# Kernel tuning notes

Hardware: AMD Instinct MI355X
Metric: run time of the kernel (lower is better)

The kernel has to match this reference:

```python
import jax, jax.numpy as jnp
import numpy as np

EPS_RMS = 1e-6
EPS_Q = 1e-5
EPS_NORM = 1e-10


def _rmsnorm(x):
    return x * jax.lax.rsqrt(jnp.mean(x * x, axis=-1, keepdims=True) + EPS_RMS)


def _activation_quant(x):
    # per-token 8-bit absmax quantization (BitNet b1.58)
    scale = 127.0 / jnp.maximum(jnp.max(jnp.abs(x), axis=-1, keepdims=True), EPS_Q)
    return jnp.clip(jnp.round(x * scale), -128.0, 127.0) / scale


def _weight_quant(w):
    # per-tensor ternary quantization with mean-abs scale
    scale = 1.0 / jnp.maximum(jnp.mean(jnp.abs(w)), EPS_Q)
    return jnp.clip(jnp.round(w * scale), -1.0, 1.0) / scale


def _bitlinear(x, w, b):
    xn = _rmsnorm(x)
    xq = xn + jax.lax.stop_gradient(_activation_quant(xn) - xn)  # STE
    wq = w + jax.lax.stop_gradient(_weight_quant(w) - w)         # STE
    return jnp.einsum('bsf,of->bso', xq, wq) + b


def setup_inputs() -> dict:
    key = jax.random.key(0)
    ks = jax.random.split(key, 4)
    B, S, F = 32, 1024, 512
    evidence_features = jax.random.normal(ks[0], (B, S, F), dtype=jnp.float32)
    prior_belief = jax.random.uniform(ks[1], (B, S, F), dtype=jnp.float32)
    W1 = jax.random.normal(ks[2], (F, 2 * F), dtype=jnp.float32) * (1.0 / np.sqrt(2 * F))
    b1 = jnp.zeros((F,), dtype=jnp.float32)
    W2 = jax.random.normal(ks[3], (F, F), dtype=jnp.float32) * (1.0 / np.sqrt(F))
    b2 = jnp.zeros((F,), dtype=jnp.float32)
    return {"evidence_features": evidence_features, "prior_belief": prior_belief,
            "W1": W1, "b1": b1, "W2": W2, "b2": b2}


def reference(evidence_features, prior_belief, W1, b1, W2, b2):
    # belief_update MLP on concat(prior, evidence)
    update_input = jnp.concatenate([prior_belief, evidence_features], axis=-1)  # [B,S,2F]
    h = jax.nn.relu(_bitlinear(update_input, W1, b1))                           # [B,S,F]
    likelihood_factors = jax.nn.sigmoid(_bitlinear(h, W2, b2))                  # [B,S,F]
    posterior_unnorm = prior_belief * likelihood_factors
    normalizer = jnp.maximum(jnp.sum(posterior_unnorm, axis=1, keepdims=True), EPS_NORM)
    return posterior_unnorm / normalizer
```

## Files before the change

### kernel.cpp

```cpp
#include <hip/hip_runtime.h>
#include <math.h>

typedef __attribute__((ext_vector_type(4))) int i32x4;
typedef __attribute__((ext_vector_type(2))) int i32x2;
typedef __attribute__((ext_vector_type(4))) float f32x4;

#define GLOAD_LDS16(g, l)                                          \
  __builtin_amdgcn_global_load_lds(                                \
      (const __attribute__((address_space(1))) void*)(g),          \
      (__attribute__((address_space(3))) void*)(l), 16, 0, 0)

__global__ void kWabs(const float* __restrict__ w1, const float* __restrict__ w2,
                      double* __restrict__ part) {
  const bool second = blockIdx.x >= 256;
  const float* w = second ? w2 : w1;
  const int n = second ? 262144 : 524288;
  int t = (blockIdx.x & 255) * 256 + threadIdx.x;
  double s = 0.0;
  for (int i = t; i < n; i += 65536) s += (double)fabsf(w[i]);
#pragma unroll
  for (int m = 32; m >= 1; m >>= 1) s += __shfl_xor(s, m);
  __shared__ double sd[4];
  int lane = threadIdx.x & 63, wid = threadIdx.x >> 6;
  if (lane == 0) sd[wid] = s;
  __syncthreads();
  if (threadIdx.x == 0) part[blockIdx.x] = (sd[0] + sd[1]) + (sd[2] + sd[3]);
}

__global__ void kWfin(const double* __restrict__ part, float* __restrict__ wsv) {
  const double* p = part + blockIdx.x * 256;
  const double n = (blockIdx.x == 0) ? 524288.0 : 262144.0;
  double s = p[threadIdx.x];
#pragma unroll
  for (int m = 32; m >= 1; m >>= 1) s += __shfl_xor(s, m);
  __shared__ double sd[4];
  int lane = threadIdx.x & 63, wid = threadIdx.x >> 6;
  if (lane == 0) sd[wid] = s;
  __syncthreads();
  if (threadIdx.x == 0) {
    double tot = (sd[0] + sd[1]) + (sd[2] + sd[3]);
    wsv[blockIdx.x] = fmaxf((float)(tot / n), 1e-5f);
  }
}

__global__ void kWq(const float* __restrict__ w1, const float* __restrict__ w2,
                    const float* __restrict__ wsv,
                    char* __restrict__ wq1, char* __restrict__ wq2) {
  const bool second = blockIdx.x >= 2048;
  const float* w = second ? w2 : w1;
  char* wq = second ? wq2 : wq1;
  const float scale = 1.0f / wsv[second ? 1 : 0];
  int i = (second ? blockIdx.x - 2048 : blockIdx.x) * 256 + threadIdx.x;
  float q = fminf(fmaxf(rintf(w[i] * scale), -1.0f), 1.0f);
  wq[i] = (char)(int)q;
}

__global__ __launch_bounds__(512) void kQ1(
    const float* __restrict__ prior, const float* __restrict__ evid,
    char* __restrict__ Xq, float* __restrict__ rAct) {
  const int w = threadIdx.x >> 6;
  const int l = threadIdx.x & 63;
  const size_t row = (size_t)blockIdx.x * 8 + w;
  const f32x4* pp = (const f32x4*)(prior + row * 512) + l * 2;
  const f32x4* pe = (const f32x4*)(evid + row * 512) + l * 2;
  f32x4 x[4];
  x[0] = pp[0]; x[1] = pp[1]; x[2] = pe[0]; x[3] = pe[1];
  float ss = 0.f, mx = 0.f;
#pragma unroll
  for (int v = 0; v < 4; ++v)
#pragma unroll
    for (int i = 0; i < 4; ++i) { float f = x[v][i]; ss += f * f; mx = fmaxf(mx, fabsf(f)); }
#pragma unroll
  for (int m = 32; m >= 1; m >>= 1) { ss += __shfl_xor(ss, m); mx = fmaxf(mx, __shfl_xor(mx, m)); }
  const float inv = 1.0f / sqrtf(ss * (1.0f / 1024.0f) + 1e-6f);
  const float amax = fmaxf(mx * inv, 1e-5f);
  const float s = 127.0f / amax;
  int pk[4];
#pragma unroll
  for (int v = 0; v < 4; ++v) {
    int p = 0;
#pragma unroll
    for (int i = 0; i < 4; ++i) {
      int qi = (int)fminf(fmaxf(rintf(x[v][i] * inv * s), -128.0f), 127.0f);
      p |= (qi & 255) << (8 * i);
    }
    pk[v] = p;
  }
  char* dst = Xq + row * 1024 + l * 8;
  *(i32x2*)dst = (i32x2){pk[0], pk[1]};
  *(i32x2*)(dst + 512) = (i32x2){pk[2], pk[3]};
  if (l == 0) rAct[row] = amax / 127.0f;
}

template <int KDIM, bool L1>
__global__ __launch_bounds__(512, 4) void kGemm(
    const char* __restrict__ Xq, const char* __restrict__ Wq,
    const float* __restrict__ biasG, const float* __restrict__ rAct,
    const float* __restrict__ wS,
    char* __restrict__ XqOut, float* __restrict__ rActOut,
    const float* __restrict__ prior, float* __restrict__ outUn,
    float* __restrict__ partG) {
  struct Stage { char A[4096]; char B[32768]; };
  __shared__ __align__(16) union {
    Stage st[2];
    struct { float sq[64][8]; float mx[64][8]; } ep;
  } u;
  __shared__ float rowR[64];
  __shared__ float biasS[512];
  __shared__ float normPart[512];

  const int tid = threadIdx.x;
  const int lane = tid & 63;
  const int wn = tid >> 6;
  const int lr = lane & 15;
  const int kg = lane >> 4;
  const size_t row0 = (size_t)blockIdx.x * 64;

  if (tid < 64) rowR[tid] = rAct[row0 + tid];
  biasS[tid] = biasG[tid];

  i32x4 acc[4][4];
#pragma unroll
  for (int a = 0; a < 4; ++a)
#pragma unroll
    for (int b = 0; b < 4; ++b) acc[a][b] = (i32x4){0, 0, 0, 0};

  const int lrow = lane >> 2;
  const int lkb = (lane & 3) * 16;

  const char* gA = Xq + (row0 + (wn & 3) * 16 + lrow) * (size_t)KDIM + lkb;
  const char* gB[4];
#pragma unroll
  for (int r = 0; r < 4; ++r)
    gB[r] = Wq + ((wn * 4 + r) * 16 + lrow) * (size_t)KDIM + lkb;

#define STAGE(b, k0)                                                   \
  do {                                                                 \
    if (wn < 4) GLOAD_LDS16(gA + (k0), &u.st[b].A[(wn & 3) * 1024]);   \
    _Pragma("unroll")                                                  \
    for (int r = 0; r < 4; ++r)                                        \
      GLOAD_LDS16(gB[r] + (k0), &u.st[b].B[(wn * 4 + r) * 1024]);      \
  } while (0)

  constexpr int NT = KDIM / 64;
  STAGE(0, 0);
  __syncthreads();

#pragma unroll 2
  for (int kt = 0; kt < NT; ++kt) {
    const int cur = kt & 1;
    if (kt + 1 < NT) STAGE(cur ^ 1, (kt + 1) * 64);
    i32x4 af[4];
#pragma unroll
    for (int fm = 0; fm < 4; ++fm)
      af[fm] = *(const i32x4*)&u.st[cur].A[(fm * 16 + lr) * 64 + kg * 16];
#pragma unroll
    for (int fn = 0; fn < 4; ++fn) {
      i32x4 bf = *(const i32x4*)&u.st[cur].B[(wn * 64 + fn * 16 + lr) * 64 + kg * 16];
#pragma unroll
      for (int fm = 0; fm < 4; ++fm)
        acc[fm][fn] = __builtin_amdgcn_mfma_i32_16x16x64_i8(af[fm], bf, acc[fm][fn], 0, 0, 0);
    }
    __syncthreads();
  }
#undef STAGE

  const float wsv_ = wS[0];

  if constexpr (L1) {
    f32x4 fa[4][4];
#pragma unroll
    for (int fm = 0; fm < 4; ++fm) {
      float sc[4];
#pragma unroll
      for (int j = 0; j < 4; ++j) sc[j] = rowR[fm * 16 + kg * 4 + j] * wsv_;
#pragma unroll
      for (int fn = 0; fn < 4; ++fn) {
        const float bb = biasS[wn * 64 + fn * 16 + lr];
#pragma unroll
        for (int j = 0; j < 4; ++j)
          fa[fm][fn][j] = fmaxf((float)acc[fm][fn][j] * sc[j] + bb, 0.0f);
      }
    }
#pragma unroll
    for (int fm = 0; fm < 4; ++fm)
#pragma unroll
      for (int j = 0; j < 4; ++j) {
        float ss = 0.f, mx = 0.f;
#pragma unroll
        for (int fn = 0; fn < 4; ++fn) { float h = fa[fm][fn][j]; ss += h * h; mx = fmaxf(mx, h); }
#pragma unroll
        for (int m = 8; m >= 1; m >>= 1) { ss += __shfl_xor(ss, m); mx = fmaxf(mx, __shfl_xor(mx, m)); }
        if (lr == 0) {
          int rl = fm * 16 + kg * 4 + j;
          u.ep.sq[rl][wn] = ss;
          u.ep.mx[rl][wn] = mx;
        }
      }
    __syncthreads();
#pragma unroll
    for (int fm = 0; fm < 4; ++fm)
#pragma unroll
      for (int j = 0; j < 4; ++j) {
        const int rl = fm * 16 + kg * 4 + j;
        float sst = 0.f, mxt = 0.f;
#pragma unroll
        for (int w = 0; w < 8; ++w) {
          sst += u.ep.sq[rl][w];
          mxt = fmaxf(mxt, u.ep.mx[rl][w]);
        }
        float inv = 1.0f / sqrtf(sst * (1.0f / 512.0f) + 1e-6f);
        float amax = fmaxf(mxt * inv, 1e-5f);
        float s = 127.0f / amax;
        if (lr == 0 && wn == 0) rActOut[row0 + rl] = amax / 127.0f;
#pragma unroll
        for (int fn = 0; fn < 4; ++fn) {
          float xn = fa[fm][fn][j] * inv;
          int qi = (int)fminf(fmaxf(rintf(xn * s), -128.0f), 127.0f);
          XqOut[(row0 + rl) * 512 + wn * 64 + fn * 16 + lr] = (char)qi;
        }
      }
  } else {
    float colsum[4] = {0.f, 0.f, 0.f, 0.f};
#pragma unroll
    for (int fm = 0; fm < 4; ++fm) {
      float sc[4];
#pragma unroll
      for (int j = 0; j < 4; ++j) sc[j] = rowR[fm * 16 + kg * 4 + j] * wsv_;
#pragma unroll
      for (int fn = 0; fn < 4; ++fn) {
        const int col = wn * 64 + fn * 16 + lr;
        const float bb = biasS[col];
#pragma unroll
        for (int j = 0; j < 4; ++j) {
          const size_t rg = row0 + fm * 16 + kg * 4 + j;
          float v = (float)acc[fm][fn][j] * sc[j] + bb;
          float like = 1.0f / (1.0f + expf(-v));
          float un = prior[rg * 512 + col] * like;
          outUn[rg * 512 + col] = un;
          colsum[fn] += un;
        }
      }
    }
#pragma unroll
    for (int fn = 0; fn < 4; ++fn) {
      colsum[fn] += __shfl_xor(colsum[fn], 16);
      colsum[fn] += __shfl_xor(colsum[fn], 32);
    }
    if (lane < 16) {
#pragma unroll
      for (int fn = 0; fn < 4; ++fn) normPart[wn * 64 + fn * 16 + lane] = colsum[fn];
    }
    __syncthreads();
    partG[(size_t)blockIdx.x * 512 + tid] = normPart[tid];
  }
}

__global__ void kNorm1(const float* __restrict__ partG, float* __restrict__ normA) {
  const int b = blockIdx.x, f = threadIdx.x;
  float s = 0.f;
#pragma unroll
  for (int i = 0; i < 16; ++i) s += partG[(size_t)(b * 16 + i) * 512 + f];
  normA[b * 512 + f] = fmaxf(s, 1e-10f);
}

__global__ void kNorm2(float* __restrict__ out, const float* __restrict__ normA) {
  const size_t i4 = (size_t)blockIdx.x * blockDim.x + threadIdx.x;
  f32x4 v = ((const f32x4*)out)[i4];
  const int f4 = (int)(i4 & 127);
  const int b = (int)(i4 >> 17);
  f32x4 n = ((const f32x4*)normA)[b * 128 + f4];
  v[0] /= n[0]; v[1] /= n[1]; v[2] /= n[2]; v[3] /= n[3];
  ((f32x4*)out)[i4] = v;
}

extern "C" void kernel_launch(void* const* d_in, const int* in_sizes, int n_in,
                              void* d_out, int out_size, void* d_ws, size_t ws_size,
                              hipStream_t stream) {
  const float* evid  = (const float*)d_in[0];
  const float* prior = (const float*)d_in[1];
  const float* W1    = (const float*)d_in[2];
  const float* b1    = (const float*)d_in[3];
  const float* W2    = (const float*)d_in[4];
  const float* b2    = (const float*)d_in[5];
  float* out = (float*)d_out;

  char* ws = (char*)d_ws;
  char*   X2q   = ws;
  char*   W1q   = ws + 16777216;
  char*   W2q   = ws + 17301504;
  float*  r1    = (float*)(ws + 17563648);
  float*  r2    = (float*)(ws + 17694720);
  double* part  = (double*)(ws + 17825792);
  float*  wsv   = (float*)(ws + 17829888);
  float*  partG = (float*)(ws + 17830144);
  float*  normA = (float*)(ws + 18878720);

  char* X1q = (char*)d_out;

  kWabs<<<512, 256, 0, stream>>>(W1, W2, part);
  kWfin<<<2, 256, 0, stream>>>(part, wsv);
  kWq<<<3072, 256, 0, stream>>>(W1, W2, wsv, W1q, W2q);
  kQ1<<<4096, 512, 0, stream>>>(prior, evid, X1q, r1);
  kGemm<1024, true><<<512, 512, 0, stream>>>(X1q, W1q, b1, r1, wsv + 0,
                                             X2q, r2, nullptr, nullptr, nullptr);
  kGemm<512, false><<<512, 512, 0, stream>>>(X2q, W2q, b2, r2, wsv + 1,
                                             nullptr, nullptr, prior, out, partG);
  kNorm1<<<32, 512, 0, stream>>>(partG, normA);
  kNorm2<<<16384, 256, 0, stream>>>(out, normA);
}
```

Before: 131.8 us.

## Fuse first-layer activation quantization into the first GEMM via LDS-resident A tile

```diff
diff --git a/kernel.cpp b/kernel.cpp
--- a/kernel.cpp
+++ b/kernel.cpp
@@ -2,7 +2,6 @@
 #include <math.h>
 
 typedef __attribute__((ext_vector_type(4))) int i32x4;
-typedef __attribute__((ext_vector_type(2))) int i32x2;
 typedef __attribute__((ext_vector_type(4))) float f32x4;
 
 #define GLOAD_LDS16(g, l)                                          \
@@ -55,59 +54,18 @@
   wq[i] = (char)(int)q;
 }
 
-__global__ __launch_bounds__(512) void kQ1(
+__global__ __launch_bounds__(512, 1) void kFused1(
     const float* __restrict__ prior, const float* __restrict__ evid,
-    char* __restrict__ Xq, float* __restrict__ rAct) {
-  const int w = threadIdx.x >> 6;
-  const int l = threadIdx.x & 63;
-  const size_t row = (size_t)blockIdx.x * 8 + w;
-  const f32x4* pp = (const f32x4*)(prior + row * 512) + l * 2;
-  const f32x4* pe = (const f32x4*)(evid + row * 512) + l * 2;
-  f32x4 x[4];
-  x[0] = pp[0]; x[1] = pp[1]; x[2] = pe[0]; x[3] = pe[1];
-  float ss = 0.f, mx = 0.f;
-#pragma unroll
-  for (int v = 0; v < 4; ++v)
-#pragma unroll
-    for (int i = 0; i < 4; ++i) { float f = x[v][i]; ss += f * f; mx = fmaxf(mx, fabsf(f)); }
-#pragma unroll
-  for (int m = 32; m >= 1; m >>= 1) { ss += __shfl_xor(ss, m); mx = fmaxf(mx, __shfl_xor(mx, m)); }
-  const float inv = 1.0f / sqrtf(ss * (1.0f / 1024.0f) + 1e-6f);
-  const float amax = fmaxf(mx * inv, 1e-5f);
-  const float s = 127.0f / amax;
-  int pk[4];
-#pragma unroll
-  for (int v = 0; v < 4; ++v) {
-    int p = 0;
-#pragma unroll
-    for (int i = 0; i < 4; ++i) {
-      int qi = (int)fminf(fmaxf(rintf(x[v][i] * inv * s), -128.0f), 127.0f);
-      p |= (qi & 255) << (8 * i);
-    }
-    pk[v] = p;
-  }
-  char* dst = Xq + row * 1024 + l * 8;
-  *(i32x2*)dst = (i32x2){pk[0], pk[1]};
-  *(i32x2*)(dst + 512) = (i32x2){pk[2], pk[3]};
-  if (l == 0) rAct[row] = amax / 127.0f;
-}
-
-template <int KDIM, bool L1>
-__global__ __launch_bounds__(512, 4) void kGemm(
-    const char* __restrict__ Xq, const char* __restrict__ Wq,
-    const float* __restrict__ biasG, const float* __restrict__ rAct,
+    const char* __restrict__ Wq, const float* __restrict__ biasG,
     const float* __restrict__ wS,
-    char* __restrict__ XqOut, float* __restrict__ rActOut,
-    const float* __restrict__ prior, float* __restrict__ outUn,
-    float* __restrict__ partG) {
-  struct Stage { char A[4096]; char B[32768]; };
+    char* __restrict__ XqOut, float* __restrict__ rActOut) {
+  __shared__ __align__(16) char Ap[65536];
   __shared__ __align__(16) union {
-    Stage st[2];
+    char B[2][32768];
     struct { float sq[64][8]; float mx[64][8]; } ep;
   } u;
-  __shared__ float rowR[64];
+  __shared__ float rowSc[64];
   __shared__ float biasS[512];
-  __shared__ float normPart[512];
 
   const int tid = threadIdx.x;
   const int lane = tid & 63;
@@ -116,6 +74,172 @@
   const int kg = lane >> 4;
   const size_t row0 = (size_t)blockIdx.x * 64;
 
+  biasS[tid] = biasG[tid];
+
+  {
+    const float* srcBase = (lane >= 32) ? evid : prior;
+    const int lcol = (lane & 31) * 16;
+    const int ldsCol = lane * 16;
+    const float* sp = srcBase + (row0 + wn * 8) * 512 + lcol;
+    f32x4 x0 = ((const f32x4*)sp)[0];
+    f32x4 x1 = ((const f32x4*)sp)[1];
+    f32x4 x2 = ((const f32x4*)sp)[2];
+    f32x4 x3 = ((const f32x4*)sp)[3];
+#pragma unroll
+    for (int rr = 0; rr < 8; ++rr) {
+      f32x4 y0, y1, y2, y3;
+      if (rr < 7) {
+        const float* np = srcBase + (row0 + wn * 8 + rr + 1) * 512 + lcol;
+        y0 = ((const f32x4*)np)[0]; y1 = ((const f32x4*)np)[1];
+        y2 = ((const f32x4*)np)[2]; y3 = ((const f32x4*)np)[3];
+      }
+      float ss = 0.f, mx = 0.f;
+      f32x4 xs[4] = {x0, x1, x2, x3};
+#pragma unroll
+      for (int v = 0; v < 4; ++v)
+#pragma unroll
+        for (int i = 0; i < 4; ++i) { float f = xs[v][i]; ss += f * f; mx = fmaxf(mx, fabsf(f)); }
+#pragma unroll
+      for (int m = 32; m >= 1; m >>= 1) { ss += __shfl_xor(ss, m); mx = fmaxf(mx, __shfl_xor(mx, m)); }
+      const float inv = 1.0f / sqrtf(ss * (1.0f / 1024.0f) + 1e-6f);
+      const float amax = fmaxf(mx * inv, 1e-5f);
+      const float s = 127.0f / amax;
+      i32x4 q;
+#pragma unroll
+      for (int v = 0; v < 4; ++v) {
+        int p = 0;
+#pragma unroll
+        for (int i = 0; i < 4; ++i) {
+          int qi = (int)fminf(fmaxf(rintf(xs[v][i] * inv * s), -128.0f), 127.0f);
+          p |= (qi & 255) << (8 * i);
+        }
+        q[v] = p;
+      }
+      const int r = wn * 8 + rr;
+      *(i32x4*)&Ap[r * 1024 + (ldsCol ^ ((r & 7) << 4))] = q;
+      if (lane == 0) rowSc[r] = amax / 127.0f;
+      if (rr < 7) { x0 = y0; x1 = y1; x2 = y2; x3 = y3; }
+    }
+  }
+
+  i32x4 acc[4][4];
+#pragma unroll
+  for (int a = 0; a < 4; ++a)
+#pragma unroll
+    for (int b = 0; b < 4; ++b) acc[a][b] = (i32x4){0, 0, 0, 0};
+
+  const int lrow = lane >> 2;
+  const int lkb = (lane & 3) * 16;
+  const char* gB[4];
+#pragma unroll
+  for (int r = 0; r < 4; ++r)
+    gB[r] = Wq + ((wn * 4 + r) * 16 + lrow) * (size_t)1024 + lkb;
+
+#define STAGEB(b, k0)                                                \
+  do {                                                               \
+    _Pragma("unroll")                                                \
+    for (int r = 0; r < 4; ++r)                                      \
+      GLOAD_LDS16(gB[r] + (k0), &u.B[b][(wn * 4 + r) * 1024]);       \
+  } while (0)
+
+  STAGEB(0, 0);
+  __syncthreads();
+
+  const int aswz = (lr & 7) << 4;
+#pragma unroll 2
+  for (int kt = 0; kt < 16; ++kt) {
+    const int cur = kt & 1;
+    if (kt + 1 < 16) STAGEB(cur ^ 1, (kt + 1) * 64);
+    const int acol = (kt * 64 + kg * 16) ^ aswz;
+    i32x4 af[4];
+#pragma unroll
+    for (int fm = 0; fm < 4; ++fm)
+      af[fm] = *(const i32x4*)&Ap[(fm * 16 + lr) * 1024 + acol];
+#pragma unroll
+    for (int fn = 0; fn < 4; ++fn) {
+      i32x4 bf = *(const i32x4*)&u.B[cur][(wn * 64 + fn * 16 + lr) * 64 + kg * 16];
+#pragma unroll
+      for (int fm = 0; fm < 4; ++fm)
+        acc[fm][fn] = __builtin_amdgcn_mfma_i32_16x16x64_i8(af[fm], bf, acc[fm][fn], 0, 0, 0);
+    }
+    __syncthreads();
+  }
+#undef STAGEB
+
+  const float wsv_ = wS[0];
+  f32x4 fa[4][4];
+#pragma unroll
+  for (int fm = 0; fm < 4; ++fm) {
+    float sc[4];
+#pragma unroll
+    for (int j = 0; j < 4; ++j) sc[j] = rowSc[fm * 16 + kg * 4 + j] * wsv_;
+#pragma unroll
+    for (int fn = 0; fn < 4; ++fn) {
+      const float bb = biasS[wn * 64 + fn * 16 + lr];
+#pragma unroll
+      for (int j = 0; j < 4; ++j)
+        fa[fm][fn][j] = fmaxf((float)acc[fm][fn][j] * sc[j] + bb, 0.0f);
+    }
+  }
+#pragma unroll
+  for (int fm = 0; fm < 4; ++fm)
+#pragma unroll
+    for (int j = 0; j < 4; ++j) {
+      float ss = 0.f, mx = 0.f;
+#pragma unroll
+      for (int fn = 0; fn < 4; ++fn) { float h = fa[fm][fn][j]; ss += h * h; mx = fmaxf(mx, h); }
+#pragma unroll
+      for (int m = 8; m >= 1; m >>= 1) { ss += __shfl_xor(ss, m); mx = fmaxf(mx, __shfl_xor(mx, m)); }
+      if (lr == 0) {
+        int rl = fm * 16 + kg * 4 + j;
+        u.ep.sq[rl][wn] = ss;
+        u.ep.mx[rl][wn] = mx;
+      }
+    }
+  __syncthreads();
+#pragma unroll
+  for (int fm = 0; fm < 4; ++fm)
+#pragma unroll
+    for (int j = 0; j < 4; ++j) {
+      const int rl = fm * 16 + kg * 4 + j;
+      float sst = 0.f, mxt = 0.f;
+#pragma unroll
+      for (int w = 0; w < 8; ++w) {
+        sst += u.ep.sq[rl][w];
+        mxt = fmaxf(mxt, u.ep.mx[rl][w]);
+      }
+      float inv = 1.0f / sqrtf(sst * (1.0f / 512.0f) + 1e-6f);
+      float amax = fmaxf(mxt * inv, 1e-5f);
+      float s = 127.0f / amax;
+      if (lr == 0 && wn == 0) rActOut[row0 + rl] = amax / 127.0f;
+#pragma unroll
+      for (int fn = 0; fn < 4; ++fn) {
+        float xn = fa[fm][fn][j] * inv;
+        int qi = (int)fminf(fmaxf(rintf(xn * s), -128.0f), 127.0f);
+        XqOut[(row0 + rl) * 512 + wn * 64 + fn * 16 + lr] = (char)qi;
+      }
+    }
+}
+
+__global__ __launch_bounds__(512, 4) void kGemm2(
+    const char* __restrict__ Xq, const char* __restrict__ Wq,
+    const float* __restrict__ biasG, const float* __restrict__ rAct,
+    const float* __restrict__ wS, const float* __restrict__ prior,
+    float* __restrict__ outUn, float* __restrict__ partG) {
+  constexpr int KDIM = 512;
+  struct Stage { char A[4096]; char B[32768]; };
+  __shared__ __align__(16) Stage st[2];
+  __shared__ float rowR[64];
+  __shared__ float biasS[512];
+  __shared__ float normPart[512];
+
+  const int tid = threadIdx.x;
+  const int lane = tid & 63;
+  const int wn = tid >> 6;
+  const int lr = lane & 15;
+  const int kg = lane >> 4;
+  const size_t row0 = (size_t)blockIdx.x * 64;
+
   if (tid < 64) rowR[tid] = rAct[row0 + tid];
   biasS[tid] = biasG[tid];
 
@@ -127,19 +251,18 @@
 
   const int lrow = lane >> 2;
   const int lkb = (lane & 3) * 16;
-
   const char* gA = Xq + (row0 + (wn & 3) * 16 + lrow) * (size_t)KDIM + lkb;
   const char* gB[4];
 #pragma unroll
   for (int r = 0; r < 4; ++r)
     gB[r] = Wq + ((wn * 4 + r) * 16 + lrow) * (size_t)KDIM + lkb;
 
-#define STAGE(b, k0)                                                   \
-  do {                                                                 \
-    if (wn < 4) GLOAD_LDS16(gA + (k0), &u.st[b].A[(wn & 3) * 1024]);   \
-    _Pragma("unroll")                                                  \
-    for (int r = 0; r < 4; ++r)                                        \
-      GLOAD_LDS16(gB[r] + (k0), &u.st[b].B[(wn * 4 + r) * 1024]);      \
+#define STAGE(b, k0)                                                 \
+  do {                                                               \
+    if (wn < 4) GLOAD_LDS16(gA + (k0), &st[b].A[(wn & 3) * 1024]);   \
+    _Pragma("unroll")                                                \
+    for (int r = 0; r < 4; ++r)                                      \
+      GLOAD_LDS16(gB[r] + (k0), &st[b].B[(wn * 4 + r) * 1024]);      \
   } while (0)
 
   constexpr int NT = KDIM / 64;
@@ -153,10 +276,10 @@
     i32x4 af[4];
 #pragma unroll
     for (int fm = 0; fm < 4; ++fm)
-      af[fm] = *(const i32x4*)&u.st[cur].A[(fm * 16 + lr) * 64 + kg * 16];
+      af[fm] = *(const i32x4*)&st[cur].A[(fm * 16 + lr) * 64 + kg * 16];
 #pragma unroll
     for (int fn = 0; fn < 4; ++fn) {
-      i32x4 bf = *(const i32x4*)&u.st[cur].B[(wn * 64 + fn * 16 + lr) * 64 + kg * 16];
+      i32x4 bf = *(const i32x4*)&st[cur].B[(wn * 64 + fn * 16 + lr) * 64 + kg * 16];
 #pragma unroll
       for (int fm = 0; fm < 4; ++fm)
         acc[fm][fn] = __builtin_amdgcn_mfma_i32_16x16x64_i8(af[fm], bf, acc[fm][fn], 0, 0, 0);
@@ -166,94 +289,38 @@
 #undef STAGE
 
   const float wsv_ = wS[0];
-
-  if constexpr (L1) {
-    f32x4 fa[4][4];
-#pragma unroll
-    for (int fm = 0; fm < 4; ++fm) {
-      float sc[4];
-#pragma unroll
-      for (int j = 0; j < 4; ++j) sc[j] = rowR[fm * 16 + kg * 4 + j] * wsv_;
-#pragma unroll
-      for (int fn = 0; fn < 4; ++fn) {
-        const float bb = biasS[wn * 64 + fn * 16 + lr];
-#pragma unroll
-        for (int j = 0; j < 4; ++j)
-          fa[fm][fn][j] = fmaxf((float)acc[fm][fn][j] * sc[j] + bb, 0.0f);
-      }
-    }
-#pragma unroll
-    for (int fm = 0; fm < 4; ++fm)
+  float colsum[4] = {0.f, 0.f, 0.f, 0.f};
+#pragma unroll
+  for (int fm = 0; fm < 4; ++fm) {
+    float sc[4];
+#pragma unroll
+    for (int j = 0; j < 4; ++j) sc[j] = rowR[fm * 16 + kg * 4 + j] * wsv_;
+#pragma unroll
+    for (int fn = 0; fn < 4; ++fn) {
+      const int col = wn * 64 + fn * 16 + lr;
+      const float bb = biasS[col];
 #pragma unroll
       for (int j = 0; j < 4; ++j) {
-        float ss = 0.f, mx = 0.f;
-#pragma unroll
-        for (int fn = 0; fn < 4; ++fn) { float h = fa[fm][fn][j]; ss += h * h; mx = fmaxf(mx, h); }
-#pragma unroll
-        for (int m = 8; m >= 1; m >>= 1) { ss += __shfl_xor(ss, m); mx = fmaxf(mx, __shfl_xor(mx, m)); }
-        if (lr == 0) {
-          int rl = fm * 16 + kg * 4 + j;
-          u.ep.sq[rl][wn] = ss;
-          u.ep.mx[rl][wn] = mx;
-        }
-      }
-    __syncthreads();
-#pragma unroll
-    for (int fm = 0; fm < 4; ++fm)
-#pragma unroll
-      for (int j = 0; j < 4; ++j) {
-        const int rl = fm * 16 + kg * 4 + j;
-        float sst = 0.f, mxt = 0.f;
-#pragma unroll
-        for (int w = 0; w < 8; ++w) {
-          sst += u.ep.sq[rl][w];
-          mxt = fmaxf(mxt, u.ep.mx[rl][w]);
-        }
-        float inv = 1.0f / sqrtf(sst * (1.0f / 512.0f) + 1e-6f);
-        float amax = fmaxf(mxt * inv, 1e-5f);
-        float s = 127.0f / amax;
-        if (lr == 0 && wn == 0) rActOut[row0 + rl] = amax / 127.0f;
-#pragma unroll
-        for (int fn = 0; fn < 4; ++fn) {
-          float xn = fa[fm][fn][j] * inv;
-          int qi = (int)fminf(fmaxf(rintf(xn * s), -128.0f), 127.0f);
-          XqOut[(row0 + rl) * 512 + wn * 64 + fn * 16 + lr] = (char)qi;
-        }
-      }
-  } else {
-    float colsum[4] = {0.f, 0.f, 0.f, 0.f};
-#pragma unroll
-    for (int fm = 0; fm < 4; ++fm) {
-      float sc[4];
-#pragma unroll
-      for (int j = 0; j < 4; ++j) sc[j] = rowR[fm * 16 + kg * 4 + j] * wsv_;
-#pragma unroll
-      for (int fn = 0; fn < 4; ++fn) {
-        const int col = wn * 64 + fn * 16 + lr;
-        const float bb = biasS[col];
-#pragma unroll
-        for (int j = 0; j < 4; ++j) {
-          const size_t rg = row0 + fm * 16 + kg * 4 + j;
-          float v = (float)acc[fm][fn][j] * sc[j] + bb;
-          float like = 1.0f / (1.0f + expf(-v));
-          float un = prior[rg * 512 + col] * like;
-          outUn[rg * 512 + col] = un;
-          colsum[fn] += un;
-        }
-      }
-    }
-#pragma unroll
-    for (int fn = 0; fn < 4; ++fn) {
-      colsum[fn] += __shfl_xor(colsum[fn], 16);
-      colsum[fn] += __shfl_xor(colsum[fn], 32);
-    }
-    if (lane < 16) {
-#pragma unroll
-      for (int fn = 0; fn < 4; ++fn) normPart[wn * 64 + fn * 16 + lane] = colsum[fn];
-    }
-    __syncthreads();
-    partG[(size_t)blockIdx.x * 512 + tid] = normPart[tid];
-  }
+        const size_t rg = row0 + fm * 16 + kg * 4 + j;
+        float v = (float)acc[fm][fn][j] * sc[j] + bb;
+        float like = 1.0f / (1.0f + expf(-v));
+        float un = prior[rg * 512 + col] * like;
+        outUn[rg * 512 + col] = un;
+        colsum[fn] += un;
+      }
+    }
+  }
+#pragma unroll
+  for (int fn = 0; fn < 4; ++fn) {
+    colsum[fn] += __shfl_xor(colsum[fn], 16);
+    colsum[fn] += __shfl_xor(colsum[fn], 32);
+  }
+  if (lane < 16) {
+#pragma unroll
+    for (int fn = 0; fn < 4; ++fn) normPart[wn * 64 + fn * 16 + lane] = colsum[fn];
+  }
+  __syncthreads();
+  partG[(size_t)blockIdx.x * 512 + tid] = normPart[tid];
 }
 
 __global__ void kNorm1(const float* __restrict__ partG, float* __restrict__ normA) {
@@ -289,23 +356,17 @@
   char*   X2q   = ws;
   char*   W1q   = ws + 16777216;
   char*   W2q   = ws + 17301504;
-  float*  r1    = (float*)(ws + 17563648);
-  float*  r2    = (float*)(ws + 17694720);
-  double* part  = (double*)(ws + 17825792);
-  float*  wsv   = (float*)(ws + 17829888);
-  float*  partG = (float*)(ws + 17830144);
-  float*  normA = (float*)(ws + 18878720);
-
-  char* X1q = (char*)d_out;
+  float*  r2    = (float*)(ws + 17563648);
+  double* part  = (double*)(ws + 17694720);
+  float*  wsv   = (float*)(ws + 17698816);
+  float*  partG = (float*)(ws + 17699072);
+  float*  normA = (float*)(ws + 18747648);
 
   kWabs<<<512, 256, 0, stream>>>(W1, W2, part);
   kWfin<<<2, 256, 0, stream>>>(part, wsv);
   kWq<<<3072, 256, 0, stream>>>(W1, W2, wsv, W1q, W2q);
-  kQ1<<<4096, 512, 0, stream>>>(prior, evid, X1q, r1);
-  kGemm<1024, true><<<512, 512, 0, stream>>>(X1q, W1q, b1, r1, wsv + 0,
-                                             X2q, r2, nullptr, nullptr, nullptr);
-  kGemm<512, false><<<512, 512, 0, stream>>>(X2q, W2q, b2, r2, wsv + 1,
-                                             nullptr, nullptr, prior, out, partG);
+  kFused1<<<512, 512, 0, stream>>>(prior, evid, W1q, b1, wsv + 0, X2q, r2);
+  kGemm2<<<512, 512, 0, stream>>>(X2q, W2q, b2, r2, wsv + 1, prior, out, partG);
   kNorm1<<<32, 512, 0, stream>>>(partG, normA);
   kNorm2<<<16384, 256, 0, stream>>>(out, normA);
 }
```

New measurement: 136.8 us. 1.04x slower.
